# Optimization experiments

Hardware: AMD Instinct MI355X
Metric: run time of the kernel (lower is better)

The kernel has to match this reference:

```python
import jax, jax.numpy as jnp
import numpy as np

B, S, NGB, NG, DIM = 64, 4096, 13, 48, 3
NCH = [8, 8, 1]
NSHELLS = 8


def setup_inputs() -> dict:
    key = jax.random.key(0)
    ks = jax.random.split(key, 16)
    rng = np.random.default_rng(0)
    # valid row-wise permutations of the N_ngb neighbor slots per group op
    GnnPerms = jnp.asarray(np.argsort(rng.random((NG, NGB)), axis=1), dtype=jnp.int64)
    NNSites = jax.random.randint(ks[0], (NGB, S), 0, S, dtype=jnp.int64)
    SitesToShells = jax.random.randint(ks[1], (S,), 0, NSHELLS, dtype=jnp.int64)
    # block-diagonal (Ng*dim, Ng*dim) cartesian rotation blocks
    blk = rng.normal(size=(NG, DIM, DIM)).astype(np.float32) * 0.5
    gd = np.zeros((NG * DIM, NG * DIM), np.float32)
    for g in range(NG):
        gd[g * DIM:(g + 1) * DIM, g * DIM:(g + 1) * DIM] = blk[g]
    gdiags = jnp.asarray(gd)
    std = 0.2
    return {
        "InStates": jax.random.normal(ks[2], (B, 1, S), jnp.float32),
        "Psi0": jax.random.normal(ks[3], (NCH[0], 1, NGB), jnp.float32) * std,
        "bias0": jax.random.normal(ks[4], (NCH[0], 1), jnp.float32) * std,
        "Psi1": jax.random.normal(ks[5], (NCH[1], NCH[0], NGB), jnp.float32) * std,
        "bias1": jax.random.normal(ks[6], (NCH[1], 1), jnp.float32) * std,
        "Psi2": jax.random.normal(ks[7], (NCH[2], NCH[1], NGB), jnp.float32) * std,
        "bias2": jax.random.normal(ks[8], (NCH[2], 1), jnp.float32) * std,
        "wtVC": jax.random.normal(ks[9], (DIM, NGB), jnp.float32) * std,
        "ShellWeights": jax.random.normal(ks[10], (NSHELLS,), jnp.float32) * std,
        "gdiags": gdiags,
        "GnnPerms": GnnPerms,
        "NNSites": NNSites,
        "SitesToShells": SitesToShells,
    }


def _rearrange(x, NNSites):
    # x: (B, Nch, S) -> (B, Nch*N_ngb, S); subchannel j of channel c holds x[b, c, NNSites[j, s]]
    b, c, s = x.shape
    return x[:, :, NNSites].reshape(b, c * NGB, s)


def _gconv(x, W, b):
    # x: (B, NchIn*N_ngb, S); W: (NchOut, NchIn, N_ngb); b: (NchOut, 1)
    # group-rotated weights: GW[o, g, c*N_ngb+j] = W[o, c, GnnPerms[g, j]]
    GW = _gconv.GW_cache  # set per-call below via closure-free pattern; replaced in reference
    raise NotImplementedError


def reference(InStates, Psi0, bias0, Psi1, bias1, Psi2, bias2, wtVC,
              ShellWeights, gdiags, GnnPerms, NNSites, SitesToShells):
    act = jax.nn.softplus

    def gconv(x, W, b):
        # rotated weights: (NchOut, Ng, NchIn*N_ngb)
        GW = W[:, :, GnnPerms].transpose(0, 2, 1, 3).reshape(W.shape[0], NG, -1)
        h = jnp.einsum('ogk,bks->bogs', GW, x) + b[:, :, None]  # (B, NchOut, Ng, S)
        return act(h).mean(axis=2)                               # group-orbit average

    out = _rearrange(InStates, NNSites)
    for W, b in ((Psi0, bias0), (Psi1, bias1), (Psi2, bias2)):
        out = gconv(out, W, b)                 # (B, NchOut, S)
        out = _rearrange(out, NNSites)         # (B, NchOut*N_ngb, S)
    # vector channel: row g*dim+d of P is wtVC[d, GnnPerms[g]]
    P = wtVC[:, GnnPerms].transpose(1, 0, 2).reshape(NG * DIM, NGB)
    Wvc = gdiags @ P                           # (Ng*dim, N_ngb)
    v = jnp.einsum('kn,bns->bks', Wvc, out)    # (B, Ng*dim, S)
    v = v.reshape(-1, NG, DIM, out.shape[-1]).mean(axis=1)  # (B, dim, S)
    v = v * ShellWeights[SitesToShells]        # per-site shell weighting
    return v.sum(axis=2) / out.shape[-1]       # (B, dim)
```

## Files before the change

### kernel.cpp

```cpp
#include <hip/hip_runtime.h>
#include <hip/hip_bf16.h>

#define BATCH 64
#define SITES 4096
#define NGB 13
#define NGRP 48
#define SDIM 3

typedef __bf16 bf16x8 __attribute__((ext_vector_type(8)));
typedef float  f32x4  __attribute__((ext_vector_type(4)));

#define OFF_AVC  0
#define OFF_U    64
#define OFF_A0   67648
#define OFF_A1   2164800
#define OFF_PART 4261952
#define UW0H 0
#define UW0L 12288
#define UW1H 24576
#define UW1L 73728
#define UW2H 122880
#define UW2L 129024

__device__ __forceinline__ float softplus_f(float h) {
    return fmaxf(h, 0.f) + __logf(1.f + __expf(-fabsf(h)));
}

__global__ __launch_bounds__(256) void precompute_kernel(
    const float* __restrict__ Psi0, const float* __restrict__ Psi1,
    const float* __restrict__ Psi2, const float* __restrict__ wtVC,
    const float* __restrict__ gdiags, const int* __restrict__ perms,
    float* __restrict__ ws)
{
    float*  Avc = ws + OFF_AVC;
    __bf16* U   = (__bf16*)(ws + OFF_U);
    int t = blockIdx.x * 256 + threadIdx.x;
    if (t < 12288) {
        int k = t & 31, row = t >> 5;
        int o = row / NGRP, g = row - o * NGRP;
        float w = (k < NGB) ? Psi0[o * NGB + perms[g * NGB + k]] : 0.f;
        __bf16 hi = (__bf16)w;
        U[UW0H + t] = hi;
        U[UW0L + t] = (__bf16)(w - (float)hi);
    } else if (t < 61440) {
        int u = t - 12288;
        int k = u & 127, row = u >> 7;
        int o = row / NGRP, g = row - o * NGRP;
        float w = 0.f;
        if (k < 104) { int j = k >> 3, c = k & 7;
                       w = Psi1[(o * 8 + c) * NGB + perms[g * NGB + j]]; }
        __bf16 hi = (__bf16)w;
        U[UW1H + u] = hi;
        U[UW1L + u] = (__bf16)(w - (float)hi);
    } else if (t < 67584) {
        int u = t - 61440;
        int k = u & 127, g = u >> 7;
        float w = 0.f;
        if (k < 104) { int j = k >> 3, c = k & 7;
                       w = Psi2[c * NGB + perms[g * NGB + j]]; }
        __bf16 hi = (__bf16)w;
        U[UW2H + u] = hi;
        U[UW2L + u] = (__bf16)(w - (float)hi);
    } else if (t < 67584 + 39 * NGRP) {
        int t2 = t - 67584;
        int g = t2 % NGRP, u = t2 / NGRP;
        int d = u / NGB, n = u % NGB;
        const int row = g * SDIM + d;
        float s = 0.f;
        for (int k = 0; k < NGRP * SDIM; k++) {
            int g2 = k / SDIM, d2 = k - g2 * SDIM;
            float p = wtVC[d2 * NGB + perms[g2 * NGB + n]];
            s = fmaf(gdiags[row * (NGRP * SDIM) + k], p, s);
        }
        atomicAdd(&Avc[u], s * (1.f / 48.f));
    }
}

template<int NCIN, int NCTOT, int CT, int KPAD, int KSTR, int NWAVES, int NWN,
         int CHUNKS>
__global__ __launch_bounds__(NWAVES * 64, 4) void layer_mfma(
    const float* __restrict__ prev,
    const __bf16* __restrict__ Wh,
    const __bf16* __restrict__ Wl,
    const float* __restrict__ bias,
    const int*   __restrict__ NN,
    float* __restrict__ out)
{
    constexpr int NTHR   = NWAVES * 64;
    constexpr int M      = NCTOT * NGRP;
    constexpr int MTILES = M / 16, NTILES = CT / 16;
    constexpr int NWM    = NWAVES / NWN;
    constexpr int MT_W   = MTILES / NWM, NT_W = NTILES / NWN;
    constexpr int KT     = KPAD / 32;
    constexpr int GS     = NGB * CT;
    constexpr int SPT    = (GS + NTHR - 1) / NTHR;
    constexpr int CPB    = SITES / CT;
    constexpr int BUF    = CT * KSTR;
    constexpr int BPB    = CPB / CHUNKS;
    constexpr int NXCD   = 8;
    constexpr int BAT_X  = BATCH / NXCD;

    static_assert(MT_W * 16 == NGRP, "wave covers exactly one o");
    static_assert(NWM * MT_W == MTILES && NWN * NT_W == NTILES, "");
    static_assert((KPAD & 31) == 0 && (KSTR & 7) == 0, "");
    static_assert(CPB % CHUNKS == 0, "block stays within one batch");
    static_assert(BATCH % NXCD == 0 && (BATCH * BPB) % NXCD == 0, "");

    __shared__ __bf16 xh_lds[2 * BUF];
    __shared__ __bf16 xl_lds[2 * BUF];

    const int tid  = threadIdx.x;
    const int wave = tid >> 6, lane = tid & 63;
    const int m16  = lane & 15, quad = lane >> 4;

    const int bid   = blockIdx.x;
    const int xcd   = bid & (NXCD - 1);
    const int slot  = bid >> 3;
    const int b     = xcd * BAT_X + slot / BPB;
    const int octet = slot % BPB;
    const int s0base = octet * (CHUNKS * CT);

    int sj[SPT], scol[SPT];
    bool sv[SPT];
#pragma unroll
    for (int i = 0; i < SPT; i++) {
        int site = tid + i * NTHR;
        sv[i] = (site < GS);
        int ss = sv[i] ? site : 0;
        sj[i] = ss / CT;
        scol[i] = ss % CT;
    }

    if constexpr (NCIN == 1) {
        for (int e = tid; e < 2 * CT * (KPAD - NGB); e += NTHR) {
            int buf = e / (CT * (KPAD - NGB));
            int r   = e % (CT * (KPAD - NGB));
            int col = r / (KPAD - NGB), p = r % (KPAD - NGB);
            xh_lds[buf * BUF + col * KSTR + NGB + p] = (__bf16)0.f;
            xl_lds[buf * BUF + col * KSTR + NGB + p] = (__bf16)0.f;
        }
    } else {
        const bf16x8 z8 = {};
        for (int e = tid; e < 2 * CT * 3; e += NTHR) {
            int buf = e / (CT * 3);
            int r   = e % (CT * 3);
            int col = r % CT, z = r / CT;
            *(bf16x8*)(xh_lds + buf * BUF + col * KSTR + 104 + z * 8) = z8;
            *(bf16x8*)(xl_lds + buf * BUF + col * KSTR + 104 + z * 8) = z8;
        }
    }

#pragma unroll
    for (int i = 0; i < SPT; i++) if (sv[i]) {
        int nn = NN[sj[i] * SITES + s0base + scol[i]];
        if constexpr (NCIN == 1) {
            float v = prev[(size_t)b * SITES + nn];
            __bf16 hi = (__bf16)v;
            xh_lds[scol[i] * KSTR + sj[i]] = hi;
            xl_lds[scol[i] * KSTR + sj[i]] = (__bf16)(v - (float)hi);
        } else {
            const float4* p4 = (const float4*)(prev + ((size_t)(b * SITES + nn)) * 8);
            float4 u0 = p4[0], u1 = p4[1];
            float v[8] = {u0.x, u0.y, u0.z, u0.w, u1.x, u1.y, u1.z, u1.w};
            bf16x8 hv, lv;
#pragma unroll
            for (int c8 = 0; c8 < 8; c8++) {
                __bf16 hi = (__bf16)v[c8];
                hv[c8] = hi;
                lv[c8] = (__bf16)(v[c8] - (float)hi);
            }
            *(bf16x8*)(xh_lds + scol[i] * KSTR + sj[i] * 8) = hv;
            *(bf16x8*)(xl_lds + scol[i] * KSTR + sj[i] * 8) = lv;
        }
    }

    int nnA[SPT];
    if (CHUNKS > 1) {
        const int s1 = s0base + CT;
#pragma unroll
        for (int i = 0; i < SPT; i++)
            nnA[i] = sv[i] ? NN[sj[i] * SITES + s1 + scol[i]] : 0;
    }
    __syncthreads();

    const int wave_mt0 = (wave / NWN) * MT_W;
    const int wave_nt0 = (wave % NWN) * NT_W;
    const int o_g      = (wave_mt0 * 16) / NGRP;
    const float bo     = bias[o_g];

#pragma unroll 1
    for (int c = 0; c < CHUNKS; c++) {
        const int cur = c & 1;

        float4 ga[SPT], gb[SPT];
        float  g1[SPT];
        if (c + 1 < CHUNKS) {
#pragma unroll
            for (int i = 0; i < SPT; i++) if (sv[i]) {
                if constexpr (NCIN == 1) {
                    g1[i] = prev[(size_t)b * SITES + nnA[i]];
                } else {
                    const float4* p4 =
                        (const float4*)(prev + ((size_t)(b * SITES + nnA[i])) * 8);
                    ga[i] = p4[0];
                    gb[i] = p4[1];
                }
            }
        }
        int nnB[SPT];
        if (c + 2 < CHUNKS) {
            const int s2 = s0base + (c + 2) * CT;
#pragma unroll
            for (int i = 0; i < SPT; i++)
                nnB[i] = sv[i] ? NN[sj[i] * SITES + s2 + scol[i]] : 0;
        }

        const __bf16* xh = xh_lds + cur * BUF;
        const __bf16* xl = xl_lds + cur * BUF;

        f32x4 acc[MT_W][NT_W];
#pragma unroll
        for (int mt = 0; mt < MT_W; mt++)
#pragma unroll
            for (int nt = 0; nt < NT_W; nt++) acc[mt][nt] = (f32x4){0.f, 0.f, 0.f, 0.f};

#pragma unroll
        for (int kt = 0; kt < KT; kt++) {
            const int koff = kt * 32 + quad * 8;
            bf16x8 ah[MT_W], al[MT_W], bh[NT_W], bl[NT_W];
#pragma unroll
            for (int mt = 0; mt < MT_W; mt++) {
                int row = (wave_mt0 + mt) * 16 + m16;
                ah[mt] = *(const bf16x8*)(Wh + (size_t)row * KPAD + koff);
                al[mt] = *(const bf16x8*)(Wl + (size_t)row * KPAD + koff);
            }
#pragma unroll
            for (int nt = 0; nt < NT_W; nt++) {
                int cbase = ((wave_nt0 + nt) * 16 + m16) * KSTR + koff;
                bh[nt] = *(const bf16x8*)(xh + cbase);
                bl[nt] = *(const bf16x8*)(xl + cbase);
            }
#pragma unroll
            for (int mt = 0; mt < MT_W; mt++)
#pragma unroll
                for (int nt = 0; nt < NT_W; nt++) {
                    acc[mt][nt] = __builtin_amdgcn_mfma_f32_16x16x32_bf16(
                        ah[mt], bh[nt], acc[mt][nt], 0, 0, 0);
                    acc[mt][nt] = __builtin_amdgcn_mfma_f32_16x16x32_bf16(
                        al[mt], bh[nt], acc[mt][nt], 0, 0, 0);
                    acc[mt][nt] = __builtin_amdgcn_mfma_f32_16x16x32_bf16(
                        ah[mt], bl[nt], acc[mt][nt], 0, 0, 0);
                }
        }

        const int s0c = s0base + c * CT;
#pragma unroll
        for (int nt = 0; nt < NT_W; nt++) {
            float s = 0.f;
#pragma unroll
            for (int mt = 0; mt < MT_W; mt++)
#pragma unroll
                for (int r = 0; r < 4; r++)
                    s += softplus_f(acc[mt][nt][r] + bo);
            s += __shfl_xor(s, 16);
            s += __shfl_xor(s, 32);
            if (quad == 0)
                out[((size_t)(b * SITES + s0c + (wave_nt0 + nt) * 16 + m16)) * NCTOT + o_g]
                    = s * (1.f / 48.f);
        }

        if (c + 1 < CHUNKS) {
            __bf16* dh = xh_lds + (cur ^ 1) * BUF;
            __bf16* dl = xl_lds + (cur ^ 1) * BUF;
#pragma unroll
            for (int i = 0; i < SPT; i++) if (sv[i]) {
                if constexpr (NCIN == 1) {
                    float v = g1[i];
                    __bf16 hi = (__bf16)v;
                    dh[scol[i] * KSTR + sj[i]] = hi;
                    dl[scol[i] * KSTR + sj[i]] = (__bf16)(v - (float)hi);
                } else {
                    float v[8] = {ga[i].x, ga[i].y, ga[i].z, ga[i].w,
                                  gb[i].x, gb[i].y, gb[i].z, gb[i].w};
                    bf16x8 hv, lv;
#pragma unroll
                    for (int c8 = 0; c8 < 8; c8++) {
                        __bf16 hi = (__bf16)v[c8];
                        hv[c8] = hi;
                        lv[c8] = (__bf16)(v[c8] - (float)hi);
                    }
                    *(bf16x8*)(dh + scol[i] * KSTR + sj[i] * 8) = hv;
                    *(bf16x8*)(dl + scol[i] * KSTR + sj[i] * 8) = lv;
                }
            }
#pragma unroll
            for (int i = 0; i < SPT; i++) nnA[i] = nnB[i];
        }
        __syncthreads();
    }
}

__global__ __launch_bounds__(256) void reduce_a(
    const float* __restrict__ A2, const int* __restrict__ NN,
    const int* __restrict__ s2sh, const float* __restrict__ sw,
    const float* __restrict__ Avc, float* __restrict__ partial)
{
    const int b = blockIdx.x >> 4;
    const int chunk = blockIdx.x & 15;
    const int tid = threadIdx.x;
    const int s = (chunk << 8) + tid;
    const float* a = A2 + (size_t)b * SITES;

    float y0 = 0.f, y1 = 0.f, y2 = 0.f;
#pragma unroll
    for (int n = 0; n < NGB; n++) {
        float v = a[NN[n * SITES + s]];
        y0 = fmaf(Avc[n],           v, y0);
        y1 = fmaf(Avc[NGB + n],     v, y1);
        y2 = fmaf(Avc[2 * NGB + n], v, y2);
    }
    const float wgt = sw[s2sh[s]];
    y0 *= wgt; y1 *= wgt; y2 *= wgt;

    __shared__ float red[3][256];
    red[0][tid] = y0; red[1][tid] = y1; red[2][tid] = y2;
    __syncthreads();
    for (int st = 128; st > 0; st >>= 1) {
        if (tid < st) {
            red[0][tid] += red[0][tid + st];
            red[1][tid] += red[1][tid + st];
            red[2][tid] += red[2][tid + st];
        }
        __syncthreads();
    }
    if (tid < 3) partial[(b * 16 + chunk) * 3 + tid] = red[tid][0];
}

__global__ __launch_bounds__(256) void reduce_b(
    const float* __restrict__ partial, float* __restrict__ out)
{
    int t = threadIdx.x;
    if (t < BATCH * 3) {
        int b = t / 3, d = t - b * 3;
        float s = 0.f;
        for (int c = 0; c < 16; c++) s += partial[(b * 16 + c) * 3 + d];
        out[t] = s * (1.f / (float)SITES);
    }
}

extern "C" void kernel_launch(void* const* d_in, const int* in_sizes, int n_in,
                              void* d_out, int out_size, void* d_ws, size_t ws_size,
                              hipStream_t stream)
{
    const float* InStates = (const float*)d_in[0];
    const float* Psi0     = (const float*)d_in[1];
    const float* bias0    = (const float*)d_in[2];
    const float* Psi1     = (const float*)d_in[3];
    const float* bias1    = (const float*)d_in[4];
    const float* Psi2     = (const float*)d_in[5];
    const float* bias2    = (const float*)d_in[6];
    const float* wtVC     = (const float*)d_in[7];
    const float* ShellW   = (const float*)d_in[8];
    const float* gdiags   = (const float*)d_in[9];
    const int*   GnnPerms = (const int*)d_in[10];
    const int*   NNSites  = (const int*)d_in[11];
    const int*   S2Sh     = (const int*)d_in[12];

    float*  ws   = (float*)d_ws;
    float*  Avc  = ws + OFF_AVC;
    __bf16* U    = (__bf16*)(ws + OFF_U);
    float*  A0   = ws + OFF_A0;
    float*  A1   = ws + OFF_A1;
    float*  A2   = ws + OFF_A0;
    float*  PART = ws + OFF_PART;

    float* out = (float*)d_out;

    hipMemsetAsync(Avc, 0, 39 * sizeof(float), stream);
    precompute_kernel<<<272, 256, 0, stream>>>(Psi0, Psi1, Psi2, wtVC, gdiags,
                                               GnnPerms, ws);

    constexpr int CHUNKS = 8;
    constexpr int NBLK   = BATCH * (SITES / 64) / CHUNKS;

    layer_mfma<1, 8, 64, 32, 40, 8, 1, CHUNKS><<<NBLK, 512, 0, stream>>>(
        InStates, U + UW0H, U + UW0L, bias0, NNSites, A0);
    layer_mfma<8, 8, 64, 128, 136, 8, 1, CHUNKS><<<NBLK, 512, 0, stream>>>(
        A0, U + UW1H, U + UW1L, bias1, NNSites, A1);
    layer_mfma<8, 1, 64, 128, 136, 4, 4, CHUNKS><<<NBLK, 256, 0, stream>>>(
        A1, U + UW2H, U + UW2L, bias2, NNSites, A2);

    reduce_a<<<BATCH * 16, 256, 0, stream>>>(A2, NNSites, S2Sh, ShellW, Avc, PART);
    reduce_b<<<1, 256, 0, stream>>>(PART, out);
}
```

Before: 384.9 us.

## Assign layer blocks to work units via per-XCD atomic ticket queues

Replaces the static blockIdx-based mapping of blocks to (batch, site chunk) with dynamic tickets. Each block reads its hardware XCC id and takes a unit from that XCD's counter, falling back to other XCDs' queues once its own is exhausted. The aim is to keep each batch's data on the XCD whose L2 already holds it, even when block dispatch is not round-robin, and to balance load across XCDs. The cost is one atomic per block plus a barrier, and the counters must be zeroed by a memset every call.

New measurement: 404.4 us. 5.1% more time.

```diff
diff --git a/kernel.cpp b/kernel.cpp
--- a/kernel.cpp
+++ b/kernel.cpp
@@ -11,6 +11,7 @@
 typedef float  f32x4  __attribute__((ext_vector_type(4)));
 
 #define OFF_AVC  0
+#define OFF_QCTR 40
 #define OFF_U    64
 #define OFF_A0   67648
 #define OFF_A1   2164800
@@ -24,6 +25,12 @@
 
 __device__ __forceinline__ float softplus_f(float h) {
     return fmaxf(h, 0.f) + __logf(1.f + __expf(-fabsf(h)));
+}
+
+__device__ __forceinline__ int xcc_id() {
+    int x;
+    asm volatile("s_getreg_b32 %0, hwreg(HW_REG_XCC_ID, 0, 4)" : "=s"(x));
+    return x & 7;
 }
 
 __global__ __launch_bounds__(256) void precompute_kernel(
@@ -84,6 +91,7 @@
     const __bf16* __restrict__ Wl,
     const float* __restrict__ bias,
     const int*   __restrict__ NN,
+    int*         __restrict__ qctr,
     float* __restrict__ out)
 {
     constexpr int NTHR   = NWAVES * 64;
@@ -99,25 +107,39 @@
     constexpr int BPB    = CPB / CHUNKS;
     constexpr int NXCD   = 8;
     constexpr int BAT_X  = BATCH / NXCD;
+    constexpr int UPQ    = BAT_X * BPB;
 
     static_assert(MT_W * 16 == NGRP, "wave covers exactly one o");
     static_assert(NWM * MT_W == MTILES && NWN * NT_W == NTILES, "");
     static_assert((KPAD & 31) == 0 && (KSTR & 7) == 0, "");
     static_assert(CPB % CHUNKS == 0, "block stays within one batch");
-    static_assert(BATCH % NXCD == 0 && (BATCH * BPB) % NXCD == 0, "");
+    static_assert(NXCD * UPQ == BATCH * BPB, "tickets == blocks");
 
     __shared__ __bf16 xh_lds[2 * BUF];
     __shared__ __bf16 xl_lds[2 * BUF];
+    __shared__ int s_unit;
 
     const int tid  = threadIdx.x;
     const int wave = tid >> 6, lane = tid & 63;
     const int m16  = lane & 15, quad = lane >> 4;
 
-    const int bid   = blockIdx.x;
-    const int xcd   = bid & (NXCD - 1);
-    const int slot  = bid >> 3;
-    const int b     = xcd * BAT_X + slot / BPB;
-    const int octet = slot % BPB;
+    if (tid == 0) {
+        int xcc = xcc_id();
+        int unit = -1;
+        for (int k = 0; k < NXCD; k++) {
+            int q = (xcc + k) & (NXCD - 1);
+            int idx = atomicAdd(&qctr[q], 1);
+            if (idx < UPQ) { unit = q * UPQ + idx; break; }
+        }
+        s_unit = unit;
+    }
+    __syncthreads();
+    const int unit = s_unit;
+    if (unit < 0) return;
+    const int q      = unit / UPQ;
+    const int idx    = unit - q * UPQ;
+    const int b      = q * BAT_X + idx / BPB;
+    const int octet  = idx % BPB;
     const int s0base = octet * (CHUNKS * CT);
 
     int sj[SPT], scol[SPT];
@@ -368,6 +390,7 @@
 
     float*  ws   = (float*)d_ws;
     float*  Avc  = ws + OFF_AVC;
+    int*    QC   = (int*)(ws + OFF_QCTR);
     __bf16* U    = (__bf16*)(ws + OFF_U);
     float*  A0   = ws + OFF_A0;
     float*  A1   = ws + OFF_A1;
@@ -376,7 +399,7 @@
 
     float* out = (float*)d_out;
 
-    hipMemsetAsync(Avc, 0, 39 * sizeof(float), stream);
+    hipMemsetAsync(ws, 0, 64 * sizeof(float), stream);
     precompute_kernel<<<272, 256, 0, stream>>>(Psi0, Psi1, Psi2, wtVC, gdiags,
                                                GnnPerms, ws);
 
@@ -384,11 +407,11 @@
     constexpr int NBLK   = BATCH * (SITES / 64) / CHUNKS;
 
     layer_mfma<1, 8, 64, 32, 40, 8, 1, CHUNKS><<<NBLK, 512, 0, stream>>>(
-        InStates, U + UW0H, U + UW0L, bias0, NNSites, A0);
+        InStates, U + UW0H, U + UW0L, bias0, NNSites, QC + 0, A0);
     layer_mfma<8, 8, 64, 128, 136, 8, 1, CHUNKS><<<NBLK, 512, 0, stream>>>(
-        A0, U + UW1H, U + UW1L, bias1, NNSites, A1);
+        A0, U + UW1H, U + UW1L, bias1, NNSites, QC + 8, A1);
     layer_mfma<8, 1, 64, 128, 136, 4, 4, CHUNKS><<<NBLK, 256, 0, stream>>>(
-        A1, U + UW2H, U + UW2L, bias2, NNSites, A2);
+        A1, U + UW2H, U + UW2L, bias2, NNSites, QC + 16, A2);
 
     reduce_a<<<BATCH * 16, 256, 0, stream>>>(A2, NNSites, S2Sh, ShellW, Avc, PART);
     reduce_b<<<1, 256, 0, stream>>>(PART, out);
```
